# Kernel tuning notes

Measured on AMD Instinct MI355X. Metric: run time of the kernel, lower is better.

Reference implementation:

```python
import jax, jax.numpy as jnp
import numpy as np

B, S, D, H = 16, 4096, 1024, 1024
VOCAB = 512
EMB_DIM = 3


def setup_inputs() -> dict:
    key = jax.random.key(0)
    ks = jax.random.split(key, 12)
    sd = 1.0 / np.sqrt(D)
    sh = 1.0 / np.sqrt(H)
    return {
        "hs": jax.random.normal(ks[0], (B, S, D), dtype=jnp.float32),
        "ht_k": jax.random.normal(ks[1], (B, D), dtype=jnp.float32),
        "hm_k": jax.random.normal(ks[2], (B, H), dtype=jnp.float32),
        "Ws_w": jax.random.uniform(ks[3], (H, D), jnp.float32, -sd, sd),
        "Ws_b": jax.random.uniform(ks[4], (H,), jnp.float32, -sd, sd),
        "Wt_w": jax.random.uniform(ks[5], (H, D), jnp.float32, -sd, sd),
        "Wt_b": jax.random.uniform(ks[6], (H,), jnp.float32, -sd, sd),
        "Wr_w": jax.random.uniform(ks[7], (H, H), jnp.float32, -sh, sh),
        "Wr_b": jax.random.uniform(ks[8], (H,), jnp.float32, -sh, sh),
        "We_w": jax.random.uniform(ks[9], (H,), jnp.float32, -sh, sh),
        "We_b": jax.random.uniform(ks[10], (1,), jnp.float32, -sh, sh),
        "emb_table": jax.random.normal(ks[11], (VOCAB * VOCAB, EMB_DIM), dtype=jnp.float32),
        "entity_lambda": jnp.array([0.3, 0.5, 0.2], dtype=jnp.float32),
        "hs_i": jax.random.randint(jax.random.fold_in(key, 100), (B, S), 0, VOCAB),
        "ht_k_i": jax.random.randint(jax.random.fold_in(key, 101), (B,), 0, VOCAB),
    }


def reference(hs, ht_k, hm_k, Ws_w, Ws_b, Wt_w, Wt_b, Wr_w, Wr_b, We_w, We_b,
              emb_table, entity_lambda, hs_i, ht_k_i):
    # Projections
    W_hs = jnp.einsum('bsd,hd->bsh', hs, Ws_w) + Ws_b          # [B,S,H]
    W_ht = (ht_k @ Wt_w.T + Wt_b)[:, None, :]                   # [B,1,H]
    W_hm = (hm_k @ Wr_w.T + Wr_b)[:, None, :]                   # [B,1,H]
    # Additive attention score
    W_sum = jnp.tanh(W_hs + W_ht + W_hm) @ We_w + We_b[0]       # [B,S]
    # Relative-position bias: gather then contract with lambda
    rel_pos = hs_i * VOCAB + ht_k_i[:, None]                    # [B,S]
    rel_value = emb_table[rel_pos] @ entity_lambda              # [B,S]
    W_sum = W_sum + rel_value
    # Softmax over sequence, weighted sum of projected source states
    W_softmax = jax.nn.softmax(W_sum, axis=1)                   # [B,S]
    alpha = jnp.einsum('bs,bsh->bh', W_softmax, W_hs)           # [B,H]
    return alpha
```

## Files before the change

kernel.cpp:

```cpp
#include <hip/hip_runtime.h>
#include <hip/hip_bf16.h>
#include <cstdint>
#include <cstddef>

typedef __attribute__((ext_vector_type(4))) float f32x4;
typedef __attribute__((ext_vector_type(8))) short short8;

#define S_LEN 4096
#define D_DIM 1024
#define H_DIM 1024
#define B_SZ  16
#define M_TOT (B_SZ * S_LEN)

__device__ __forceinline__ unsigned short f2bf(float f) {
  unsigned int u = __float_as_uint(f);
  u += 0x7fffu + ((u >> 16) & 1u);
  return (unsigned short)(u >> 16);
}

__device__ __forceinline__ void gload_lds16(void* lds, const void* g) {
  __builtin_amdgcn_global_load_lds(
      (const __attribute__((address_space(1))) unsigned int*)g,
      (__attribute__((address_space(3))) unsigned int*)lds, 16, 0, 0);
}

__device__ __forceinline__ float tanh_fast(float x) {
  return 1.0f - 2.0f / (1.0f + __expf(2.0f * x));
}

#define BAR() __builtin_amdgcn_s_barrier()
#define LGKM0()                                            \
  do {                                                     \
    asm volatile("s_waitcnt lgkmcnt(0)" ::: "memory");     \
    __builtin_amdgcn_sched_barrier(0);                     \
  } while (0)

__global__ void cvt_hs_kernel(const float* __restrict__ w,
                              unsigned short* __restrict__ o) {
  size_t i = ((size_t)blockIdx.x * 256 + threadIdx.x) * 8;
  float4 v0 = *(const float4*)(w + i);
  float4 v1 = *(const float4*)(w + i + 4);
  union { unsigned short us[8]; short8 v; } pk;
  pk.us[0] = f2bf(v0.x); pk.us[1] = f2bf(v0.y);
  pk.us[2] = f2bf(v0.z); pk.us[3] = f2bf(v0.w);
  pk.us[4] = f2bf(v1.x); pk.us[5] = f2bf(v1.y);
  pk.us[6] = f2bf(v1.z); pk.us[7] = f2bf(v1.w);
  *(short8*)(o + i) = pk.v;
}

__global__ void cvt_w_kernel(const float* __restrict__ w,
                             unsigned short* __restrict__ o) {
  int i = (blockIdx.x * 256 + threadIdx.x) * 8;
  float4 v0 = *(const float4*)(w + i);
  float4 v1 = *(const float4*)(w + i + 4);
  union { unsigned short us[8]; short8 v; } pk;
  pk.us[0] = f2bf(v0.x); pk.us[1] = f2bf(v0.y);
  pk.us[2] = f2bf(v0.z); pk.us[3] = f2bf(v0.w);
  pk.us[4] = f2bf(v1.x); pk.us[5] = f2bf(v1.y);
  pk.us[6] = f2bf(v1.z); pk.us[7] = f2bf(v1.w);
  *(short8*)(o + i) = pk.v;
}

__global__ void prep_c_kernel(const float* __restrict__ ht,
                              const float* __restrict__ hm,
                              const float* __restrict__ Wt_w,
                              const float* __restrict__ Wt_b,
                              const float* __restrict__ Wr_w,
                              const float* __restrict__ Wr_b,
                              float* __restrict__ cvec) {
  int gw = blockIdx.x * 4 + (threadIdx.x >> 6);
  int lane = threadIdx.x & 63;
  int b = gw >> 10;
  int h = gw & 1023;
  const float* a1 = ht + b * D_DIM;
  const float* w1 = Wt_w + (size_t)h * D_DIM;
  const float* a2 = hm + b * H_DIM;
  const float* w2 = Wr_w + (size_t)h * H_DIM;
  float acc = 0.f;
#pragma unroll
  for (int i = 0; i < 4; ++i) {
    int d = lane * 4 + i * 256;
    float4 x1 = *(const float4*)(a1 + d);
    float4 y1 = *(const float4*)(w1 + d);
    float4 x2 = *(const float4*)(a2 + d);
    float4 y2 = *(const float4*)(w2 + d);
    acc += x1.x * y1.x + x1.y * y1.y + x1.z * y1.z + x1.w * y1.w;
    acc += x2.x * y2.x + x2.y * y2.y + x2.z * y2.z + x2.w * y2.w;
  }
#pragma unroll
  for (int off = 32; off >= 1; off >>= 1) acc += __shfl_xor(acc, off);
  if (lane == 0) cvec[b * H_DIM + h] = acc + Wt_b[h] + Wr_b[h];
}

#define STG_A(nb, h, ss)                                                  \
  do {                                                                    \
    gload_lds16(lA + (nb)*16384 + (h)*8192 + dst0,                        \
                gA + (h)*131072 + (ss)*64);                               \
    gload_lds16(lA + (nb)*16384 + (h)*8192 + dst1,                        \
                gA + (h)*131072 + 65536 + (ss)*64);                       \
  } while (0)
#define STG_B(nb, h, ss)                                                  \
  do {                                                                    \
    gload_lds16(lB + (nb)*16384 + (h)*8192 + dst0,                        \
                gB + (h)*131072 + (ss)*64);                               \
    gload_lds16(lB + (nb)*16384 + (h)*8192 + dst1,                        \
                gB + (h)*131072 + 65536 + (ss)*64);                       \
  } while (0)

#define RDA_LO(OFF)                                                       \
  { _Pragma("unroll") for (int mi = 0; mi < 4; ++mi)                      \
      fa[mi] = *(const short8*)(bA + (OFF) + mi * 1024); }
#define RDA_HI(OFF)                                                       \
  { _Pragma("unroll") for (int mi = 0; mi < 4; ++mi)                      \
      fa[mi] = *(const short8*)(bA + (OFF) + 4096 + mi * 1024); }
#define RDB(FB, OFF)                                                      \
  { _Pragma("unroll") for (int ni = 0; ni < 4; ++ni)                      \
      FB[ni] = *(const short8*)(bB + (OFF) + ni * 1024); }

#define MM16(MIB, FB)                                                     \
  {                                                                       \
    __builtin_amdgcn_s_setprio(1);                                        \
    _Pragma("unroll") for (int mi = 0; mi < 4; ++mi) {                    \
      _Pragma("unroll") for (int ni = 0; ni < 4; ++ni) {                  \
        acc[(MIB) + mi][ni] = __builtin_amdgcn_mfma_f32_16x16x32_bf16(    \
            fa[mi], FB[ni], acc[(MIB) + mi][ni], 0, 0, 0);                \
      }                                                                   \
    }                                                                     \
    __builtin_amdgcn_s_setprio(0);                                        \
  }

__global__ __launch_bounds__(512, 2) void score_gemm3_kernel(
    const unsigned short* __restrict__ hsb,
    const unsigned short* __restrict__ Wsb,
    const float* __restrict__ cvec,
    const float* __restrict__ We_w,
    float* __restrict__ score_part) {
  extern __shared__ unsigned short dynls[];
  unsigned short* lA = dynls;
  unsigned short* lB = dynls + 32768;
  __shared__ float scorebuf[4][256];

  const int tid = threadIdx.x;
  const int lane = tid & 63;
  const int wave = tid >> 6;
  const int wm = wave >> 2;
  const int wn = wave & 3;
  const int l15 = lane & 15;
  const int lg = lane >> 4;

  int d = blockIdx.x;
  int tileid = (d & 7) * 128 + (d >> 3);
  const int mtile = tileid >> 2;
  const int nc = tileid & 3;
  const int m0 = mtile * 256;
  const int n0 = nc * 256;
  const int b = m0 >> 12;

  const int tr = tid >> 3;
  const int tc = tid & 7;
  const int scol = ((tc ^ (tr & 7)) << 3);
  const unsigned short* gA = hsb + (size_t)(m0 + tr) * 1024 + scol;
  const unsigned short* gB = Wsb + (size_t)(n0 + tr) * 1024 + scol;
  const int dst0 = tid * 8;
  const int dst1 = 4096 + tid * 8;

  const int aoff0 = (wm * 128 + l15) * 64 + ((lg ^ (l15 & 7)) << 3);
  const int aoff1 = (wm * 128 + l15) * 64 + (((4 + lg) ^ (l15 & 7)) << 3);
  const int boff0 = (wn * 64 + l15) * 64 + ((lg ^ (l15 & 7)) << 3);
  const int boff1 = (wn * 64 + l15) * 64 + (((4 + lg) ^ (l15 & 7)) << 3);

  f32x4 acc[8][4];
#pragma unroll
  for (int i = 0; i < 8; ++i)
#pragma unroll
    for (int j = 0; j < 4; ++j) acc[i][j] = (f32x4){0.f, 0.f, 0.f, 0.f};

  STG_A(0, 0, 0);
  STG_A(0, 1, 0);
  STG_B(0, 0, 0);
  STG_B(0, 1, 0);
  asm volatile("s_waitcnt vmcnt(0)" ::: "memory");
  BAR();

#pragma unroll 2
  for (int s = 0; s < 16; ++s) {
    const unsigned short* bA = lA + (s & 1) * 16384;
    const unsigned short* bB = lB + (s & 1) * 16384;
    const int nb = (s & 1) ^ 1;
    const bool st = (s < 15);
    short8 fa[4], fb0[4], fb1[4];
    RDA_LO(aoff0);
    RDB(fb0, boff0);
    if (st) STG_A(nb, 0, s + 1);
    BAR();
    LGKM0();
    MM16(0, fb0);
    BAR();
    RDA_HI(aoff0);
    if (st) STG_A(nb, 1, s + 1);
    BAR();
    LGKM0();
    MM16(4, fb0);
    BAR();
    RDA_LO(aoff1);
    RDB(fb1, boff1);
    if (st) STG_B(nb, 0, s + 1);
    BAR();
    LGKM0();
    MM16(0, fb1);
    BAR();
    RDA_HI(aoff1);
    if (st) STG_B(nb, 1, s + 1);
    BAR();
    LGKM0();
    MM16(4, fb1);
    asm volatile("s_waitcnt vmcnt(0)" ::: "memory");
    BAR();
  }

  float chv[4], whv[4];
#pragma unroll
  for (int ni = 0; ni < 4; ++ni) {
    int h = n0 + wn * 64 + ni * 16 + l15;
    chv[ni] = cvec[b * H_DIM + h];
    whv[ni] = We_w[h];
  }
#pragma unroll
  for (int mi = 0; mi < 8; ++mi)
#pragma unroll
    for (int r = 0; r < 4; ++r) {
      float s = 0.f;
#pragma unroll
      for (int ni = 0; ni < 4; ++ni)
        s += tanh_fast(acc[mi][ni][r] + chv[ni]) * whv[ni];
      s += __shfl_xor(s, 1);
      s += __shfl_xor(s, 2);
      s += __shfl_xor(s, 4);
      s += __shfl_xor(s, 8);
      if (l15 == 0) scorebuf[wn][wm * 128 + mi * 16 + lg * 4 + r] = s;
    }
  __syncthreads();
  if (tid < 256) {
    float s = scorebuf[0][tid] + scorebuf[1][tid] + scorebuf[2][tid] +
              scorebuf[3][tid];
    score_part[(size_t)nc * M_TOT + m0 + tid] = s;
  }
}

__global__ __launch_bounds__(256) void score_gemm_fp32_kernel(
    const float* __restrict__ hs,
    const unsigned short* __restrict__ Wsb,
    const float* __restrict__ cvec,
    const float* __restrict__ We_w,
    float* __restrict__ score_part) {
  __shared__ __align__(16) unsigned short lA[128 * 64];
  __shared__ __align__(16) unsigned short lB[128 * 64];
  __shared__ float scorebuf[2][128];

  const int tid = threadIdx.x;
  const int lane = tid & 63;
  const int wave = tid >> 6;
  const int wr = wave >> 1;
  const int wc = wave & 1;
  const int mtile = blockIdx.x;
  const int gy = blockIdx.y;
  const int m0 = mtile * 128;
  const int b = mtile >> 5;
  const int l15 = lane & 15;
  const int lg = lane >> 4;

  float rowsum[4][4];
#pragma unroll
  for (int i = 0; i < 4; ++i)
#pragma unroll
    for (int j = 0; j < 4; ++j) rowsum[i][j] = 0.f;

  for (int ncq = gy * 4; ncq < gy * 4 + 4; ++ncq) {
    const int n0 = ncq * 128;
    f32x4 acc[4][4];
#pragma unroll
    for (int i = 0; i < 4; ++i)
#pragma unroll
      for (int j = 0; j < 4; ++j) acc[i][j] = (f32x4){0.f, 0.f, 0.f, 0.f};

    for (int k0 = 0; k0 < D_DIM; k0 += 64) {
#pragma unroll
      for (int r = 0; r < 4; ++r) {
        int s = tid + r * 256;
        int row = s >> 3, sl = s & 7;
        int src = sl ^ (row & 7);
        gload_lds16(&lB[s * 8], Wsb + (size_t)(n0 + row) * D_DIM + k0 + src * 8);
      }
      float4 a0[4], a1[4];
#pragma unroll
      for (int r = 0; r < 4; ++r) {
        int s = tid + r * 256;
        int row = s >> 3, sl = s & 7;
        int src = sl ^ (row & 7);
        const float* ga = hs + (size_t)(m0 + row) * D_DIM + k0 + src * 8;
        a0[r] = *(const float4*)ga;
        a1[r] = *(const float4*)(ga + 4);
      }
#pragma unroll
      for (int r = 0; r < 4; ++r) {
        int s = tid + r * 256;
        union { unsigned short us[8]; short8 v; } pk;
        pk.us[0] = f2bf(a0[r].x); pk.us[1] = f2bf(a0[r].y);
        pk.us[2] = f2bf(a0[r].z); pk.us[3] = f2bf(a0[r].w);
        pk.us[4] = f2bf(a1[r].x); pk.us[5] = f2bf(a1[r].y);
        pk.us[6] = f2bf(a1[r].z); pk.us[7] = f2bf(a1[r].w);
        *(short8*)(&lA[s * 8]) = pk.v;
      }
      __syncthreads();
#pragma unroll
      for (int kf = 0; kf < 2; ++kf) {
        short8 af[4], bfr[4];
        int cgrp = kf * 4 + lg;
#pragma unroll
        for (int mi = 0; mi < 4; ++mi) {
          int row = wr * 64 + mi * 16 + l15;
          af[mi] = *(const short8*)&lA[row * 64 + (cgrp ^ (row & 7)) * 8];
        }
#pragma unroll
        for (int ni = 0; ni < 4; ++ni) {
          int row = wc * 64 + ni * 16 + l15;
          bfr[ni] = *(const short8*)&lB[row * 64 + (cgrp ^ (row & 7)) * 8];
        }
#pragma unroll
        for (int mi = 0; mi < 4; ++mi)
#pragma unroll
          for (int ni = 0; ni < 4; ++ni)
            acc[mi][ni] = __builtin_amdgcn_mfma_f32_16x16x32_bf16(
                af[mi], bfr[ni], acc[mi][ni], 0, 0, 0);
      }
      __syncthreads();
    }
#pragma unroll
    for (int ni = 0; ni < 4; ++ni) {
      int h = n0 + wc * 64 + ni * 16 + l15;
      float ch = cvec[b * H_DIM + h];
      float wh = We_w[h];
#pragma unroll
      for (int mi = 0; mi < 4; ++mi)
#pragma unroll
        for (int r2 = 0; r2 < 4; ++r2)
          rowsum[mi][r2] += tanh_fast(acc[mi][ni][r2] + ch) * wh;
    }
  }
#pragma unroll
  for (int mi = 0; mi < 4; ++mi)
#pragma unroll
    for (int r2 = 0; r2 < 4; ++r2) {
      float v = rowsum[mi][r2];
      v += __shfl_xor(v, 1);
      v += __shfl_xor(v, 2);
      v += __shfl_xor(v, 4);
      v += __shfl_xor(v, 8);
      rowsum[mi][r2] = v;
    }
  if (l15 == 0) {
#pragma unroll
    for (int mi = 0; mi < 4; ++mi)
#pragma unroll
      for (int r2 = 0; r2 < 4; ++r2)
        scorebuf[wc][wr * 64 + mi * 16 + lg * 4 + r2] = rowsum[mi][r2];
  }
  __syncthreads();
  if (tid < 128) {
    score_part[(size_t)gy * M_TOT + m0 + tid] =
        scorebuf[0][tid] + scorebuf[1][tid];
  }
}

__global__ void softmax_kernel(const float* __restrict__ part,
                               const int* __restrict__ hs_i,
                               const int* __restrict__ ht_i,
                               const float* __restrict__ emb,
                               const float* __restrict__ lam,
                               float* __restrict__ wout, int nparts) {
  int b = blockIdx.x;
  int tid = threadIdx.x;
  float lam0 = lam[0], lam1 = lam[1], lam2 = lam[2];
  int tk = ht_i[b];
  float xs[16];
  float mx = -1e30f;
#pragma unroll
  for (int i = 0; i < 16; ++i) {
    int s = tid + i * 256;
    size_t m = (size_t)b * S_LEN + s;
    float x = 0.f;
    for (int g = 0; g < nparts; ++g) x += part[(size_t)g * M_TOT + m];
    int idx = hs_i[m] * 512 + tk;
    const float* e = emb + (size_t)idx * 3;
    x += e[0] * lam0 + e[1] * lam1 + e[2] * lam2;
    xs[i] = x;
    mx = fmaxf(mx, x);
  }
  __shared__ float redm[4];
  __shared__ float reds[4];
#pragma unroll
  for (int off = 32; off >= 1; off >>= 1) mx = fmaxf(mx, __shfl_xor(mx, off));
  if ((tid & 63) == 0) redm[tid >> 6] = mx;
  __syncthreads();
  mx = fmaxf(fmaxf(redm[0], redm[1]), fmaxf(redm[2], redm[3]));
  float sum = 0.f;
#pragma unroll
  for (int i = 0; i < 16; ++i) {
    xs[i] = __expf(xs[i] - mx);
    sum += xs[i];
  }
#pragma unroll
  for (int off = 32; off >= 1; off >>= 1) sum += __shfl_xor(sum, off);
  if ((tid & 63) == 0) reds[tid >> 6] = sum;
  __syncthreads();
  sum = reds[0] + reds[1] + reds[2] + reds[3];
  float inv = 1.0f / sum;
#pragma unroll
  for (int i = 0; i < 16; ++i)
    wout[(size_t)b * S_LEN + tid + i * 256] = xs[i] * inv;
}

__global__ void wsum_bf16_kernel(const unsigned short* __restrict__ hsb,
                                 const float* __restrict__ w,
                                 float* __restrict__ u) {
  int bx = blockIdx.x;
  int b = bx >> 5;
  int sc = bx & 31;
  int tid = threadIdx.x;
  int dcol = tid * 4;
  int s0 = sc * 128;
  const unsigned short* base = hsb + ((size_t)b * S_LEN + s0) * D_DIM + dcol;
  const float* wrow = w + (size_t)b * S_LEN + s0;
  float4 acc = {0.f, 0.f, 0.f, 0.f};
#pragma unroll 4
  for (int i = 0; i < 128; ++i) {
    float ww = wrow[i];
    ushort2 v01 = *(const ushort2*)(base + (size_t)i * D_DIM);
    ushort2 v23 = *(const ushort2*)(base + (size_t)i * D_DIM + 2);
    acc.x += ww * __uint_as_float((unsigned int)v01.x << 16);
    acc.y += ww * __uint_as_float((unsigned int)v01.y << 16);
    acc.z += ww * __uint_as_float((unsigned int)v23.x << 16);
    acc.w += ww * __uint_as_float((unsigned int)v23.y << 16);
  }
  atomicAdd(&u[b * D_DIM + dcol + 0], acc.x);
  atomicAdd(&u[b * D_DIM + dcol + 1], acc.y);
  atomicAdd(&u[b * D_DIM + dcol + 2], acc.z);
  atomicAdd(&u[b * D_DIM + dcol + 3], acc.w);
}

__global__ void wsum_kernel(const float* __restrict__ hs,
                            const float* __restrict__ w,
                            float* __restrict__ u) {
  int bx = blockIdx.x;
  int b = bx >> 5;
  int sc = bx & 31;
  int tid = threadIdx.x;
  int dcol = tid * 4;
  int s0 = sc * 128;
  const float* base = hs + ((size_t)b * S_LEN + s0) * D_DIM + dcol;
  const float* wrow = w + (size_t)b * S_LEN + s0;
  float4 acc = {0.f, 0.f, 0.f, 0.f};
#pragma unroll 4
  for (int i = 0; i < 128; ++i) {
    float ww = wrow[i];
    float4 v = *(const float4*)(base + (size_t)i * D_DIM);
    acc.x += ww * v.x;
    acc.y += ww * v.y;
    acc.z += ww * v.z;
    acc.w += ww * v.w;
  }
  atomicAdd(&u[b * D_DIM + dcol + 0], acc.x);
  atomicAdd(&u[b * D_DIM + dcol + 1], acc.y);
  atomicAdd(&u[b * D_DIM + dcol + 2], acc.z);
  atomicAdd(&u[b * D_DIM + dcol + 3], acc.w);
}

__global__ void alpha_kernel(const float* __restrict__ u,
                             const float* __restrict__ Ws_w,
                             const float* __restrict__ Ws_b,
                             float* __restrict__ out) {
  int gw = blockIdx.x * 4 + (threadIdx.x >> 6);
  int lane = threadIdx.x & 63;
  int b = gw >> 10;
  int h = gw & 1023;
  const float* ur = u + b * D_DIM;
  const float* wrow = Ws_w + (size_t)h * D_DIM;
  float acc = 0.f;
#pragma unroll
  for (int i = 0; i < 4; ++i) {
    int dcol = lane * 4 + i * 256;
    float4 x = *(const float4*)(ur + dcol);
    float4 y = *(const float4*)(wrow + dcol);
    acc += x.x * y.x + x.y * y.y + x.z * y.z + x.w * y.w;
  }
#pragma unroll
  for (int off = 32; off >= 1; off >>= 1) acc += __shfl_xor(acc, off);
  if (lane == 0) out[b * H_DIM + h] = acc + Ws_b[h];
}

extern "C" void kernel_launch(void* const* d_in, const int* in_sizes, int n_in,
                              void* d_out, int out_size, void* d_ws,
                              size_t ws_size, hipStream_t stream) {
  const float* hs = (const float*)d_in[0];
  const float* ht_k = (const float*)d_in[1];
  const float* hm_k = (const float*)d_in[2];
  const float* Ws_w = (const float*)d_in[3];
  const float* Ws_b = (const float*)d_in[4];
  const float* Wt_w = (const float*)d_in[5];
  const float* Wt_b = (const float*)d_in[6];
  const float* Wr_w = (const float*)d_in[7];
  const float* Wr_b = (const float*)d_in[8];
  const float* We_w = (const float*)d_in[9];
  const float* emb = (const float*)d_in[11];
  const float* lam = (const float*)d_in[12];
  const int* hs_i = (const int*)d_in[13];
  const int* ht_i = (const int*)d_in[14];
  float* out = (float*)d_out;

  const size_t HSB = (size_t)M_TOT * D_DIM * 2;
  const size_t FAST_NEEDED = HSB + 2097152 + 1048576 + 262144 + 65536 + 65536;

  char* ws = (char*)d_ws;
  if (ws_size >= FAST_NEEDED) {
    unsigned short* hsb = (unsigned short*)ws;
    unsigned short* Wsb = (unsigned short*)(ws + HSB);
    float* part = (float*)(ws + HSB + 2097152);
    float* wgt = (float*)(ws + HSB + 2097152 + 1048576);
    float* u = (float*)(ws + HSB + 2097152 + 1048576 + 262144);
    float* cvec = (float*)(ws + HSB + 2097152 + 1048576 + 262144 + 65536);

    hipFuncSetAttribute((const void*)score_gemm3_kernel,
                        hipFuncAttributeMaxDynamicSharedMemorySize, 131072);

    cvt_hs_kernel<<<32768, 256, 0, stream>>>(hs, hsb);
    cvt_w_kernel<<<512, 256, 0, stream>>>(Ws_w, Wsb);
    prep_c_kernel<<<4096, 256, 0, stream>>>(ht_k, hm_k, Wt_w, Wt_b, Wr_w,
                                            Wr_b, cvec);
    score_gemm3_kernel<<<1024, 512, 131072, stream>>>(hsb, Wsb, cvec, We_w,
                                                      part);
    softmax_kernel<<<16, 256, 0, stream>>>(part, hs_i, ht_i, emb, lam, wgt, 4);
    hipMemsetAsync(u, 0, B_SZ * D_DIM * sizeof(float), stream);
    wsum_bf16_kernel<<<512, 256, 0, stream>>>(hsb, wgt, u);
    alpha_kernel<<<4096, 256, 0, stream>>>(u, Ws_w, Ws_b, out);
    return;
  }

  unsigned short* Wsb = (unsigned short*)(ws);
  float* cvec = (float*)(ws + 2097152);
  float* part = (float*)(ws + 2097152 + 65536);
  float* wgt = (float*)(ws + 2097152 + 65536 + 524288);
  float* u = (float*)(ws + 2097152 + 65536 + 524288 + 262144);

  cvt_w_kernel<<<512, 256, 0, stream>>>(Ws_w, Wsb);
  prep_c_kernel<<<4096, 256, 0, stream>>>(ht_k, hm_k, Wt_w, Wt_b, Wr_w, Wr_b,
                                          cvec);
  dim3 g2(512, 2);
  score_gemm_fp32_kernel<<<g2, 256, 0, stream>>>(hs, Wsb, cvec, We_w, part);
  softmax_kernel<<<16, 256, 0, stream>>>(part, hs_i, ht_i, emb, lam, wgt, 2);
  hipMemsetAsync(u, 0, B_SZ * D_DIM * sizeof(float), stream);
  wsum_kernel<<<512, 256, 0, stream>>>(hs, wgt, u);
  alpha_kernel<<<4096, 256, 0, stream>>>(u, Ws_w, Ws_b, out);
}
```

Measured before the change: 288.5 us.

## Restructure score GEMM staging into deeper prefetch with 32-wide K subtiles

Rewrites the score GEMM main loop so the LDS holds K=32 half-subtiles arranged to allow prefetching up to two K-steps ahead, using partial vmcnt waits instead of a full drain each iteration. The LDS layout and XOR swizzle change to 32-element rows, and launch bounds drop to one block per CU. The aim is to hide global-to-LDS latency behind MFMA work. In exchange the buffer reuse ordering becomes more intricate, which carries a risk of races, and occupancy is lower.

```diff
diff --git a/kernel.cpp b/kernel.cpp
--- a/kernel.cpp
+++ b/kernel.cpp
@@ -29,6 +29,7 @@
 }
 
 #define BAR() __builtin_amdgcn_s_barrier()
+#define WAITV(N) asm volatile("s_waitcnt vmcnt(" #N ")" ::: "memory")
 #define LGKM0()                                            \
   do {                                                     \
     asm volatile("s_waitcnt lgkmcnt(0)" ::: "memory");     \
@@ -92,52 +93,13 @@
   if (lane == 0) cvec[b * H_DIM + h] = acc + Wt_b[h] + Wr_b[h];
 }
 
-#define STG_A(nb, h, ss)                                                  \
-  do {                                                                    \
-    gload_lds16(lA + (nb)*16384 + (h)*8192 + dst0,                        \
-                gA + (h)*131072 + (ss)*64);                               \
-    gload_lds16(lA + (nb)*16384 + (h)*8192 + dst1,                        \
-                gA + (h)*131072 + 65536 + (ss)*64);                       \
-  } while (0)
-#define STG_B(nb, h, ss)                                                  \
-  do {                                                                    \
-    gload_lds16(lB + (nb)*16384 + (h)*8192 + dst0,                        \
-                gB + (h)*131072 + (ss)*64);                               \
-    gload_lds16(lB + (nb)*16384 + (h)*8192 + dst1,                        \
-                gB + (h)*131072 + 65536 + (ss)*64);                       \
-  } while (0)
-
-#define RDA_LO(OFF)                                                       \
-  { _Pragma("unroll") for (int mi = 0; mi < 4; ++mi)                      \
-      fa[mi] = *(const short8*)(bA + (OFF) + mi * 1024); }
-#define RDA_HI(OFF)                                                       \
-  { _Pragma("unroll") for (int mi = 0; mi < 4; ++mi)                      \
-      fa[mi] = *(const short8*)(bA + (OFF) + 4096 + mi * 1024); }
-#define RDB(FB, OFF)                                                      \
-  { _Pragma("unroll") for (int ni = 0; ni < 4; ++ni)                      \
-      FB[ni] = *(const short8*)(bB + (OFF) + ni * 1024); }
-
-#define MM16(MIB, FB)                                                     \
-  {                                                                       \
-    __builtin_amdgcn_s_setprio(1);                                        \
-    _Pragma("unroll") for (int mi = 0; mi < 4; ++mi) {                    \
-      _Pragma("unroll") for (int ni = 0; ni < 4; ++ni) {                  \
-        acc[(MIB) + mi][ni] = __builtin_amdgcn_mfma_f32_16x16x32_bf16(    \
-            fa[mi], FB[ni], acc[(MIB) + mi][ni], 0, 0, 0);                \
-      }                                                                   \
-    }                                                                     \
-    __builtin_amdgcn_s_setprio(0);                                        \
-  }
-
-__global__ __launch_bounds__(512, 2) void score_gemm3_kernel(
+__global__ __launch_bounds__(512, 1) void score_gemm5_kernel(
     const unsigned short* __restrict__ hsb,
     const unsigned short* __restrict__ Wsb,
     const float* __restrict__ cvec,
     const float* __restrict__ We_w,
     float* __restrict__ score_part) {
-  extern __shared__ unsigned short dynls[];
-  unsigned short* lA = dynls;
-  unsigned short* lB = dynls + 32768;
+  extern __shared__ unsigned short L[];
   __shared__ float scorebuf[4][256];
 
   const int tid = threadIdx.x;
@@ -148,26 +110,34 @@
   const int l15 = lane & 15;
   const int lg = lane >> 4;
 
-  int d = blockIdx.x;
-  int tileid = (d & 7) * 128 + (d >> 3);
+  int dd = blockIdx.x;
+  int tileid = (dd & 7) * 128 + (dd >> 3);
   const int mtile = tileid >> 2;
   const int nc = tileid & 3;
   const int m0 = mtile * 256;
   const int n0 = nc * 256;
   const int b = m0 >> 12;
 
-  const int tr = tid >> 3;
-  const int tc = tid & 7;
-  const int scol = ((tc ^ (tr & 7)) << 3);
-  const unsigned short* gA = hsb + (size_t)(m0 + tr) * 1024 + scol;
-  const unsigned short* gB = Wsb + (size_t)(n0 + tr) * 1024 + scol;
-  const int dst0 = tid * 8;
-  const int dst1 = 4096 + tid * 8;
-
-  const int aoff0 = (wm * 128 + l15) * 64 + ((lg ^ (l15 & 7)) << 3);
-  const int aoff1 = (wm * 128 + l15) * 64 + (((4 + lg) ^ (l15 & 7)) << 3);
-  const int boff0 = (wn * 64 + l15) * 64 + ((lg ^ (l15 & 7)) << 3);
-  const int boff1 = (wn * 64 + l15) * 64 + (((4 + lg) ^ (l15 & 7)) << 3);
+  const int r0 = tid >> 2;
+  const int ps = tid & 3;
+  const int c0 = ((ps ^ ((r0 >> 1) & 3)) << 3);
+  const unsigned short* gA = hsb + (size_t)(m0 + r0) * D_DIM + c0;
+  const unsigned short* gB = Wsb + (size_t)(n0 + r0) * D_DIM + c0;
+  const int dst = tid * 8;
+
+#define STG(ROFF, GSRC)                             \
+  do {                                              \
+    gload_lds16(L + (ROFF) + dst, (GSRC));          \
+    gload_lds16(L + (ROFF) + 4096 + dst, (GSRC) + 131072); \
+  } while (0)
+
+  const int aswz = ((lg ^ ((l15 >> 1) & 3)) << 3);
+  const int abase = (wm * 128 + l15) * 32 + aswz;
+  const int bbase = (wn * 64 + l15) * 32 + aswz;
+
+#define RD4(F, OFF)                                         \
+  { _Pragma("unroll") for (int q = 0; q < 4; ++q)           \
+      F[q] = *(const short8*)(L + (OFF) + q * 512); }
 
   f32x4 acc[8][4];
 #pragma unroll
@@ -175,48 +145,70 @@
 #pragma unroll
     for (int j = 0; j < 4; ++j) acc[i][j] = (f32x4){0.f, 0.f, 0.f, 0.f};
 
-  STG_A(0, 0, 0);
-  STG_A(0, 1, 0);
-  STG_B(0, 0, 0);
-  STG_B(0, 1, 0);
-  asm volatile("s_waitcnt vmcnt(0)" ::: "memory");
+#define MM16(MB, FB)                                                     \
+  {                                                                      \
+    __builtin_amdgcn_s_setprio(1);                                       \
+    _Pragma("unroll") for (int mi = 0; mi < 4; ++mi) {                   \
+      _Pragma("unroll") for (int ni = 0; ni < 4; ++ni) {                 \
+        acc[(MB) + mi][ni] = __builtin_amdgcn_mfma_f32_16x16x32_bf16(    \
+            fa[mi], FB[ni], acc[(MB) + mi][ni], 0, 0, 0);                \
+      }                                                                  \
+    }                                                                    \
+    __builtin_amdgcn_s_setprio(0);                                       \
+  }
+
+  STG(0, gA);
+  STG(8192, gA + 32);
+  STG(16384, gB);
+  STG(24576, gB + 32);
+  STG(32768 + 16384, gB + 64);
+  STG(32768, gA + 64);
+  STG(32768 + 24576, gB + 96);
+  WAITV(6);
   BAR();
 
 #pragma unroll 2
-  for (int s = 0; s < 16; ++s) {
-    const unsigned short* bA = lA + (s & 1) * 16384;
-    const unsigned short* bB = lB + (s & 1) * 16384;
-    const int nb = (s & 1) ^ 1;
-    const bool st = (s < 15);
+  for (int t = 0; t < 16; ++t) {
+    const int bo = (t & 1) << 15;
+    const int bn = ((t + 1) & 1) << 15;
+    const int g1 = (t + 1) * 64;
+    const int g2 = (t + 2) * 64;
     short8 fa[4], fb0[4], fb1[4];
-    RDA_LO(aoff0);
-    RDB(fb0, boff0);
-    if (st) STG_A(nb, 0, s + 1);
+    RD4(fb0, bo + 16384 + bbase);
+    RD4(fa, bo + abase);
+    if (t < 15) STG(bn + 8192, gA + g1 + 32);
     BAR();
     LGKM0();
     MM16(0, fb0);
     BAR();
-    RDA_HI(aoff0);
-    if (st) STG_A(nb, 1, s + 1);
+    RD4(fa, bo + abase + 2048);
+    if (t < 14) STG(bo + 16384, gB + g2);
     BAR();
     LGKM0();
     MM16(4, fb0);
     BAR();
-    RDA_LO(aoff1);
-    RDB(fb1, boff1);
-    if (st) STG_B(nb, 0, s + 1);
+    RD4(fb1, bo + 24576 + bbase);
+    RD4(fa, bo + 8192 + abase);
+    if (t < 14) STG(bo, gA + g2);
     BAR();
     LGKM0();
     MM16(0, fb1);
     BAR();
-    RDA_HI(aoff1);
-    if (st) STG_B(nb, 1, s + 1);
+    RD4(fa, bo + 8192 + abase + 2048);
+    if (t < 14) STG(bo + 24576, gB + g2 + 32);
     BAR();
     LGKM0();
     MM16(4, fb1);
-    asm volatile("s_waitcnt vmcnt(0)" ::: "memory");
-    BAR();
-  }
+    if (t < 14) {
+      WAITV(6);
+    } else if (t == 14) {
+      WAITV(0);
+    }
+    BAR();
+  }
+#undef STG
+#undef RD4
+#undef MM16
 
   float chv[4], whv[4];
 #pragma unroll
@@ -287,16 +279,16 @@
 #pragma unroll
       for (int r = 0; r < 4; ++r) {
         int s = tid + r * 256;
-        int row = s >> 3, sl = s & 7;
-        int src = sl ^ (row & 7);
+        int row = s >> 3, slx = s & 7;
+        int src = slx ^ (row & 7);
         gload_lds16(&lB[s * 8], Wsb + (size_t)(n0 + row) * D_DIM + k0 + src * 8);
       }
       float4 a0[4], a1[4];
 #pragma unroll
       for (int r = 0; r < 4; ++r) {
         int s = tid + r * 256;
-        int row = s >> 3, sl = s & 7;
-        int src = sl ^ (row & 7);
+        int row = s >> 3, slx = s & 7;
+        int src = slx ^ (row & 7);
         const float* ga = hs + (size_t)(m0 + row) * D_DIM + k0 + src * 8;
         a0[r] = *(const float4*)ga;
         a1[r] = *(const float4*)(ga + 4);
@@ -529,14 +521,14 @@
     float* u = (float*)(ws + HSB + 2097152 + 1048576 + 262144);
     float* cvec = (float*)(ws + HSB + 2097152 + 1048576 + 262144 + 65536);
 
-    hipFuncSetAttribute((const void*)score_gemm3_kernel,
+    hipFuncSetAttribute((const void*)score_gemm5_kernel,
                         hipFuncAttributeMaxDynamicSharedMemorySize, 131072);
 
     cvt_hs_kernel<<<32768, 256, 0, stream>>>(hs, hsb);
     cvt_w_kernel<<<512, 256, 0, stream>>>(Ws_w, Wsb);
     prep_c_kernel<<<4096, 256, 0, stream>>>(ht_k, hm_k, Wt_w, Wt_b, Wr_w,
                                             Wr_b, cvec);
-    score_gemm3_kernel<<<1024, 512, 131072, stream>>>(hsb, Wsb, cvec, We_w,
+    score_gemm5_kernel<<<1024, 512, 131072, stream>>>(hsb, Wsb, cvec, We_w,
                                                       part);
     softmax_kernel<<<16, 256, 0, stream>>>(part, hs_i, ht_i, emb, lam, wgt, 4);
     hipMemsetAsync(u, 0, B_SZ * D_DIM * sizeof(float), stream);
```

Result: slower. 296.7 us (+2.9%).
